# Kernel optimization log

Measured on AMD Instinct MI355X. Metric: run time of the kernel, lower is better.

The kernel has to match this reference:

```python
import jax, jax.numpy as jnp
import numpy as np

N = 100000
E = 1250000
IN_C = 64
HID = 128
OUT_C = 64
K = 10
ALPHA = 0.1


def setup_inputs() -> dict:
    key = jax.random.key(0)
    ks = jax.random.split(key, 10)
    s = 1.0 / np.sqrt(IN_C)
    sh = 1.0 / np.sqrt(HID)
    return {
        "x": jax.random.normal(ks[0], (N, IN_C), jnp.float32),
        "edge_attr": jax.random.normal(ks[1], (E, IN_C), jnp.float32),
        "W_node": jax.random.uniform(ks[2], (IN_C, HID), jnp.float32, -s, s),
        "b_node": jnp.zeros((HID,), jnp.float32),
        "W_edge": jax.random.uniform(ks[3], (IN_C, HID), jnp.float32, -s, s),
        "b_edge": jnp.zeros((HID,), jnp.float32),
        "W1": jax.random.uniform(ks[4], (HID, HID), jnp.float32, -sh, sh),
        "b1": jnp.zeros((HID,), jnp.float32),
        "W2": jax.random.uniform(ks[5], (HID, OUT_C), jnp.float32, -sh, sh),
        "b2": jnp.zeros((OUT_C,), jnp.float32),
        "edge_index": jax.random.randint(ks[6], (2, E), 0, N, jnp.int32),
    }


def _appnp(h0, edge_index):
    # PyG APPNP with gcn_norm (adds self-loops, symmetric normalization).
    src = jnp.concatenate([edge_index[0], jnp.arange(N, dtype=edge_index.dtype)])
    dst = jnp.concatenate([edge_index[1], jnp.arange(N, dtype=edge_index.dtype)])
    ew = jnp.ones(src.shape, h0.dtype)
    deg = jax.ops.segment_sum(ew, dst, num_segments=N)
    dinv = jnp.where(deg > 0, jax.lax.rsqrt(jnp.maximum(deg, 1e-12)), 0.0)
    norm = (dinv[src] * dinv[dst])[:, None]  # [(E+N),1]

    def step(h, _):
        agg = jax.ops.segment_sum(norm * h[src], dst, num_segments=N)
        return (1.0 - ALPHA) * agg + ALPHA * h0, None

    h, _ = jax.lax.scan(step, h0, None, length=K)
    return h


def reference(x, edge_attr, W_node, b_node, W_edge, b_edge, W1, b1, W2, b2, edge_index):
    x_node = x @ W_node + b_node            # [N, HID]
    e_emb = edge_attr @ W_edge + b_edge     # [E, HID]
    # add self loops with zero edge embeddings
    ar = jnp.arange(N, dtype=edge_index.dtype)
    row = jnp.concatenate([edge_index[0], ar])
    col = jnp.concatenate([edge_index[1], ar])
    e_emb_loop = jnp.concatenate([e_emb, jnp.zeros((N, HID), e_emb.dtype)], axis=0)
    msg = x_node[col] + e_emb_loop           # [(E+N), HID]
    ssum = jax.ops.segment_sum(msg, row, num_segments=N)
    cnt = jax.ops.segment_sum(jnp.ones(row.shape, x.dtype), row, num_segments=N)
    x_enh = ssum / jnp.maximum(cnt, 1.0)[:, None]  # scatter mean (cnt>=1 via loops)
    x_enh = jax.nn.relu(x_enh)               # dropout = identity in eval
    h = jax.nn.relu(x_enh @ W1 + b1)
    h0 = h @ W2 + b2                         # [N, OUT_C]
    return _appnp(h0, edge_index)
```

## Files before the change

### kernel.cpp

```cpp
#include <hip/hip_runtime.h>
#include <hip/hip_bf16.h>
#include <hip/hip_fp16.h>

#define N_NODES 100000
#define E_EDGES 1250000
#define INC 64
#define HIDC 128
#define OUTC 64
#define K_ITERS 10
#define ALPHA 0.1f

__global__ __launch_bounds__(256) void hist2(const int* __restrict__ ei,
                                             int* __restrict__ degRow,
                                             int* __restrict__ degDst) {
    int e = blockIdx.x * 256 + threadIdx.x;
    if (e >= E_EDGES) return;
    atomicAdd(&degRow[ei[e]], 1);
    atomicAdd(&degDst[ei[E_EDGES + e]], 1);
}

__global__ __launch_bounds__(256) void dinv_kernel(const int* __restrict__ degDst,
                                                   float* __restrict__ dinv) {
    int i = blockIdx.x * 256 + threadIdx.x;
    if (i >= N_NODES) return;
    dinv[i] = rsqrtf((float)(degDst[i] + 1));
}

__global__ __launch_bounds__(256) void xconvert(const float2* __restrict__ x2,
                                                __half2* __restrict__ x16) {
    int i = blockIdx.x * 256 + threadIdx.x;
    if (i >= N_NODES * 32) return;
    float2 v = x2[i];
    x16[i] = __floats2half2_rn(v.x, v.y);
}

__global__ __launch_bounds__(256) void scan_block_sums2(const int* __restrict__ degRow,
                                                        const int* __restrict__ degDst,
                                                        int* __restrict__ blockSums) {
    const int* deg = blockIdx.y ? degDst : degRow;
    __shared__ int sh[256];
    int t = threadIdx.x;
    int i = blockIdx.x * 256 + t;
    sh[t] = (i < N_NODES) ? deg[i] : 0;
    __syncthreads();
    for (int off = 128; off > 0; off >>= 1) {
        if (t < off) sh[t] += sh[t + off];
        __syncthreads();
    }
    if (t == 0) blockSums[blockIdx.y * 512 + blockIdx.x] = sh[0];
}

__global__ __launch_bounds__(512) void scan_top2(const int* __restrict__ blockSums,
                                                 int* __restrict__ blockScan, int nb) {
    const int* bs = blockSums + blockIdx.x * 512;
    int* bo = blockScan + blockIdx.x * 512;
    __shared__ int sh[512];
    int t = threadIdx.x;
    int v = (t < nb) ? bs[t] : 0;
    sh[t] = v;
    __syncthreads();
    for (int off = 1; off < 512; off <<= 1) {
        int xv = (t >= off) ? sh[t - off] : 0;
        __syncthreads();
        sh[t] += xv;
        __syncthreads();
    }
    if (t < nb) bo[t] = sh[t] - v;
}

__global__ __launch_bounds__(256) void scan_write_rp2(const int* __restrict__ degRow,
                                                      const int* __restrict__ degDst,
                                                      const int* __restrict__ blockScan,
                                                      int* __restrict__ rpRow,
                                                      int* __restrict__ rpDst) {
    const int* deg = blockIdx.y ? degDst : degRow;
    int* rp = blockIdx.y ? rpDst : rpRow;
    __shared__ int sh[256];
    int t = threadIdx.x;
    int i = blockIdx.x * 256 + t;
    int v = (i < N_NODES) ? deg[i] : 0;
    sh[t] = v;
    __syncthreads();
    for (int off = 1; off < 256; off <<= 1) {
        int xv = (t >= off) ? sh[t - off] : 0;
        __syncthreads();
        sh[t] += xv;
        __syncthreads();
    }
    if (i < N_NODES) rp[i] = blockScan[blockIdx.y * 512 + blockIdx.x] + (sh[t] - v);
    if (i == 0) rp[N_NODES] = E_EDGES;
}

__global__ __launch_bounds__(256) void scatter_both(const int* __restrict__ ei,
                                                    const float* __restrict__ dinv,
                                                    const int* __restrict__ rpRow,
                                                    const int* __restrict__ rpDst,
                                                    int* __restrict__ curRow,
                                                    int* __restrict__ curDst,
                                                    int2* __restrict__ ce,
                                                    int2* __restrict__ ew) {
    int e = blockIdx.x * 256 + threadIdx.x;
    if (e >= E_EDGES) return;
    int r0 = ei[e];
    int r1 = ei[E_EDGES + e];
    int pr = rpRow[r0] + atomicAdd(&curRow[r0], 1);
    ce[pr] = make_int2(r1, e);
    int pd = rpDst[r1] + atomicAdd(&curDst[r1], 1);
    float w = (1.0f - ALPHA) * dinv[r0] * dinv[r1];
    ew[pd] = make_int2(r0, __float_as_int(w));
}

__global__ __launch_bounds__(256) void aggregate(const float2* __restrict__ x2,
                                                 const __half2* __restrict__ x16,
                                                 const float2* __restrict__ ea2,
                                                 const int* __restrict__ rpRow,
                                                 const int2* __restrict__ ce,
                                                 float* __restrict__ S,
                                                 float* __restrict__ cntRow) {
    int wid = (blockIdx.x * 256 + threadIdx.x) >> 6;
    int lane = threadIdx.x & 63;
    if (wid >= N_NODES) return;
    int half = lane >> 5;
    int l2 = lane & 31;
    int jb = rpRow[wid], je = rpRow[wid + 1];
    float ax0 = 0.f, ay0 = 0.f, ax1 = 0.f, ay1 = 0.f;
    float ex0 = 0.f, ey0 = 0.f, ex1 = 0.f, ey1 = 0.f;
    if (!half) {
        float2 self = x2[(size_t)wid * 32 + l2];
        ax0 = self.x; ay0 = self.y;
    }
    int j = jb;
    for (; j + 3 < je; j += 4) {
        int2 c0 = ce[j + half];
        int2 c1 = ce[j + 2 + half];
        float2 xg0 = __half22float2(x16[(size_t)c0.x * 32 + l2]);
        float2 eg0 = ea2[(size_t)c0.y * 32 + l2];
        float2 xg1 = __half22float2(x16[(size_t)c1.x * 32 + l2]);
        float2 eg1 = ea2[(size_t)c1.y * 32 + l2];
        ax0 += xg0.x; ay0 += xg0.y; ex0 += eg0.x; ey0 += eg0.y;
        ax1 += xg1.x; ay1 += xg1.y; ex1 += eg1.x; ey1 += eg1.y;
    }
    for (; j < je; j += 2) {
        int ii = j + half;
        int2 c = ce[ii < je ? ii : (je - 1)];
        float m = (ii < je) ? 1.0f : 0.0f;
        float2 xg = __half22float2(x16[(size_t)c.x * 32 + l2]);
        float2 eg = ea2[(size_t)c.y * 32 + l2];
        ax0 += m * xg.x; ay0 += m * xg.y;
        ex0 += m * eg.x; ey0 += m * eg.y;
    }
    ax0 += ax1; ay0 += ay1; ex0 += ex1; ey0 += ey1;
    ax0 += __shfl_xor(ax0, 32);
    ay0 += __shfl_xor(ay0, 32);
    ex0 += __shfl_xor(ex0, 32);
    ey0 += __shfl_xor(ey0, 32);
    if (!half) {
        *reinterpret_cast<float2*>(&S[(size_t)wid * 128 + l2 * 2]) = make_float2(ax0, ay0);
        *reinterpret_cast<float2*>(&S[(size_t)wid * 128 + 64 + l2 * 2]) = make_float2(ex0, ey0);
        if (lane == 0) cntRow[wid] = (float)(je - jb + 1);
    }
}

template <int NC, int MODE>
__global__ __launch_bounds__(256) void gemm_k(const float* __restrict__ A,
                                              const float* __restrict__ Wa,
                                              const float* __restrict__ Wb,
                                              const float* __restrict__ ba,
                                              const float* __restrict__ bb,
                                              const float* __restrict__ cnt,
                                              float* __restrict__ out) {
    constexpr int CPT = NC / 16;
    __shared__ float Al[64][132];
    __shared__ float Wl[64][NC];
    const int tid = threadIdx.x;
    const int rb = blockIdx.x * 64;

    for (int idx = tid; idx < 64 * 32; idx += 256) {
        int r = idx >> 5, c4 = idx & 31;
        int gr = rb + r;
        float4 v = make_float4(0.f, 0.f, 0.f, 0.f);
        if (gr < N_NODES) v = *reinterpret_cast<const float4*>(A + (size_t)gr * 128 + c4 * 4);
        *reinterpret_cast<float4*>(&Al[r][c4 * 4]) = v;
    }

    const int trow = tid >> 4, tcol = tid & 15;
    float acc[4][CPT];
#pragma unroll
    for (int q = 0; q < 4; q++)
#pragma unroll
        for (int j = 0; j < CPT; j++) acc[q][j] = 0.f;

    for (int half = 0; half < 2; ++half) {
        __syncthreads();
        for (int idx = tid; idx < 64 * (NC / 4); idx += 256) {
            int k = idx / (NC / 4), c4 = idx % (NC / 4);
            int gk = half * 64 + k;
            const float* src;
            if constexpr (MODE == 0) {
                src = (gk < 64) ? (Wa + (size_t)gk * NC + c4 * 4)
                                : (Wb + (size_t)(gk - 64) * NC + c4 * 4);
            } else {
                src = Wa + (size_t)gk * NC + c4 * 4;
            }
            *reinterpret_cast<float4*>(&Wl[k][c4 * 4]) = *reinterpret_cast<const float4*>(src);
        }
        __syncthreads();
#pragma unroll 4
        for (int k = 0; k < 64; k++) {
            float a0 = Al[trow][half * 64 + k];
            float a1 = Al[trow + 16][half * 64 + k];
            float a2 = Al[trow + 32][half * 64 + k];
            float a3 = Al[trow + 48][half * 64 + k];
#pragma unroll
            for (int j = 0; j < CPT; j++) {
                float w = Wl[k][j * 16 + tcol];
                acc[0][j] += a0 * w;
                acc[1][j] += a1 * w;
                acc[2][j] += a2 * w;
                acc[3][j] += a3 * w;
            }
        }
    }

#pragma unroll
    for (int q = 0; q < 4; q++) {
        int gr = rb + trow + 16 * q;
        if (gr >= N_NODES) continue;
        float inv = 0.f;
        if constexpr (MODE == 0) inv = 1.0f / cnt[gr];
#pragma unroll
        for (int j = 0; j < CPT; j++) {
            int c = j * 16 + tcol;
            float v = acc[q][j];
            if constexpr (MODE == 0) {
                v = v * inv + ba[c] + (1.0f - inv) * bb[c];
                v = fmaxf(v, 0.f);
                out[(size_t)gr * NC + c] = v;
            } else if constexpr (MODE == 1) {
                v = fmaxf(v + ba[c], 0.f);
                out[(size_t)gr * NC + c] = v;
            } else {
                v = v + ba[c];
                ((__half*)out)[(size_t)gr * NC + c] = __float2half(v);
            }
        }
    }
}

template <bool LAST>
__global__ __launch_bounds__(256) void appnp_step(const __half2* __restrict__ h2,
                                                  const __half2* __restrict__ h02,
                                                  void* __restrict__ outv,
                                                  const int* __restrict__ rp,
                                                  const int2* __restrict__ ew,
                                                  const float* __restrict__ dinv) {
    int wid = (blockIdx.x * 256 + threadIdx.x) >> 6;
    int lane = threadIdx.x & 63;
    if (wid >= N_NODES) return;
    int half = lane >> 5;
    int l2 = lane & 31;
    float acc0x = 0.f, acc0y = 0.f, acc1x = 0.f, acc1y = 0.f;
    if (!half) {
        float di = dinv[wid];
        float sw = (1.0f - ALPHA) * di * di;
        float2 hv = __half22float2(h2[(size_t)wid * 32 + l2]);
        acc0x = sw * hv.x; acc0y = sw * hv.y;
    }
    int e = rp[wid], eend = rp[wid + 1];
    for (; e + 3 < eend; e += 4) {
        int2 p0 = ew[e + half];
        int2 p1 = ew[e + 2 + half];
        float w0 = __int_as_float(p0.y);
        float w1 = __int_as_float(p1.y);
        float2 g0 = __half22float2(h2[(size_t)p0.x * 32 + l2]);
        float2 g1 = __half22float2(h2[(size_t)p1.x * 32 + l2]);
        acc0x += w0 * g0.x; acc0y += w0 * g0.y;
        acc1x += w1 * g1.x; acc1y += w1 * g1.y;
    }
    for (; e < eend; e += 2) {
        int ii = e + half;
        int2 p = ew[ii < eend ? ii : (eend - 1)];
        float w0 = (ii < eend) ? __int_as_float(p.y) : 0.0f;
        float2 g = __half22float2(h2[(size_t)p.x * 32 + l2]);
        acc0x += w0 * g.x; acc0y += w0 * g.y;
    }
    acc0x += acc1x; acc0y += acc1y;
    acc0x += __shfl_xor(acc0x, 32);
    acc0y += __shfl_xor(acc0y, 32);
    if (!half) {
        float2 hz = __half22float2(h02[(size_t)wid * 32 + l2]);
        float ox = acc0x + ALPHA * hz.x;
        float oy = acc0y + ALPHA * hz.y;
        if constexpr (LAST) {
            ((float2*)outv)[(size_t)wid * 32 + l2] = make_float2(ox, oy);
        } else {
            ((__half2*)outv)[(size_t)wid * 32 + l2] = __floats2half2_rn(ox, oy);
        }
    }
}

extern "C" void kernel_launch(void* const* d_in, const int* in_sizes, int n_in,
                              void* d_out, int out_size, void* d_ws, size_t ws_size,
                              hipStream_t stream) {
    const float* x      = (const float*)d_in[0];
    const float* eattr  = (const float*)d_in[1];
    const float* W_node = (const float*)d_in[2];
    const float* b_node = (const float*)d_in[3];
    const float* W_edge = (const float*)d_in[4];
    const float* b_edge = (const float*)d_in[5];
    const float* W1     = (const float*)d_in[6];
    const float* b1     = (const float*)d_in[7];
    const float* W2     = (const float*)d_in[8];
    const float* b2     = (const float*)d_in[9];
    const int*   ei     = (const int*)d_in[10];
    float* out = (float*)d_out;

    char* ws = (char*)d_ws;
    size_t off = 0;
    auto alloc = [&](size_t bytes) -> void* {
        void* p = ws + off;
        off += (bytes + 511) & ~(size_t)511;
        return p;
    };
    float*  buf0   = (float*)alloc((size_t)N_NODES * 128 * 4);
    __half* h0_16  = (__half*)alloc((size_t)N_NODES * 64 * 2);
    __half* x16    = (__half*)alloc((size_t)N_NODES * 64 * 2);
    int2*   ew     = (int2*)alloc((size_t)E_EDGES * 8);
    float*  cntRow = (float*)alloc((size_t)N_NODES * 4);
    int*    zeros4 = (int*)alloc((size_t)4 * N_NODES * 4);
    float*  dinv   = (float*)alloc((size_t)N_NODES * 4);
    int*    rpRow  = (int*)alloc((size_t)(N_NODES + 1) * 4);
    int*    rpDst  = (int*)alloc((size_t)(N_NODES + 1) * 4);
    int*    blockSums = (int*)alloc(1024 * 4);
    int*    blockScan = (int*)alloc(1024 * 4);

    int* degRow = zeros4;
    int* degDst = zeros4 + N_NODES;
    int* curRow = zeros4 + 2 * N_NODES;
    int* curDst = zeros4 + 3 * N_NODES;

    int2* ce = (int2*)h0_16;

    constexpr int NB = (N_NODES + 255) / 256;

    hipMemsetAsync(zeros4, 0, (size_t)4 * N_NODES * 4, stream);

    hist2<<<(E_EDGES + 255) / 256, 256, 0, stream>>>(ei, degRow, degDst);
    dinv_kernel<<<(N_NODES + 255) / 256, 256, 0, stream>>>(degDst, dinv);
    xconvert<<<(N_NODES * 32 + 255) / 256, 256, 0, stream>>>((const float2*)x, (__half2*)x16);

    scan_block_sums2<<<dim3(NB, 2), 256, 0, stream>>>(degRow, degDst, blockSums);
    scan_top2<<<2, 512, 0, stream>>>(blockSums, blockScan, NB);
    scan_write_rp2<<<dim3(NB, 2), 256, 0, stream>>>(degRow, degDst, blockScan, rpRow, rpDst);

    scatter_both<<<(E_EDGES + 255) / 256, 256, 0, stream>>>(ei, dinv, rpRow, rpDst,
                                                            curRow, curDst, ce, ew);

    aggregate<<<(N_NODES + 3) / 4, 256, 0, stream>>>((const float2*)x, (const __half2*)x16,
                                                     (const float2*)eattr, rpRow, ce,
                                                     buf0, cntRow);

    gemm_k<128, 0><<<(N_NODES + 63) / 64, 256, 0, stream>>>(buf0, W_node, W_edge, b_node, b_edge, cntRow, buf0);
    gemm_k<128, 1><<<(N_NODES + 63) / 64, 256, 0, stream>>>(buf0, W1, nullptr, b1, nullptr, nullptr, buf0);
    gemm_k<64, 2><<<(N_NODES + 63) / 64, 256, 0, stream>>>(buf0, W2, nullptr, b2, nullptr, nullptr, (float*)h0_16);

    __half* hA16 = (__half*)buf0;
    __half* hB16 = (__half*)(buf0 + (size_t)N_NODES * 32);
    const __half2* hcur = (const __half2*)h0_16;
    for (int k = 0; k < K_ITERS; k++) {
        if (k == K_ITERS - 1) {
            appnp_step<true><<<(N_NODES * 64 + 255) / 256, 256, 0, stream>>>(
                hcur, (const __half2*)h0_16, (void*)out, rpDst, ew, dinv);
        } else {
            __half* dst = (k & 1) ? hB16 : hA16;
            appnp_step<false><<<(N_NODES * 64 + 255) / 256, 256, 0, stream>>>(
                hcur, (const __half2*)h0_16, (void*)dst, rpDst, ew, dinv);
            hcur = (const __half2*)dst;
        }
    }
}
```

Measured before the change: 1.097 ms.

## Replace FP32 SIMT GEMMs with FP16 MFMA kernels and half-precision intermediates

Replaces the three scalar-FMA dense layers with a matrix-core kernel built on mfma_f32_16x16x32_f16. It adds a small pre-pass that transposes and converts the weights to fp16. The aggregation output and the GEMM intermediates are now stored in half precision, which halves their memory traffic. The cost is lower precision in the MLP intermediates and three extra tiny kernel launches.

New measurement: 990.5 us (median of 2 runs). 1.11x faster.

```diff
diff --git a/kernel.cpp b/kernel.cpp
--- a/kernel.cpp
+++ b/kernel.cpp
@@ -10,6 +10,9 @@
 #define K_ITERS 10
 #define ALPHA 0.1f
 
+typedef _Float16 f16x8 __attribute__((ext_vector_type(8)));
+typedef float f32x4 __attribute__((ext_vector_type(4)));
+
 __global__ __launch_bounds__(256) void hist2(const int* __restrict__ ei,
                                              int* __restrict__ degRow,
                                              int* __restrict__ degDst) {
@@ -32,6 +35,18 @@
     if (i >= N_NODES * 32) return;
     float2 v = x2[i];
     x16[i] = __floats2half2_rn(v.x, v.y);
+}
+
+__global__ __launch_bounds__(256) void wtrans(const float* __restrict__ Wa,
+                                              const float* __restrict__ Wb,
+                                              __half* __restrict__ dst, int NC) {
+    int idx = blockIdx.x * 256 + threadIdx.x;
+    if (idx >= NC * 128) return;
+    int n = idx >> 7, k = idx & 127;
+    float v;
+    if (Wb != nullptr && k >= 64) v = Wb[(size_t)(k - 64) * NC + n];
+    else v = Wa[(size_t)k * NC + n];
+    dst[idx] = __float2half(v);
 }
 
 __global__ __launch_bounds__(256) void scan_block_sums2(const int* __restrict__ degRow,
@@ -115,7 +130,7 @@
                                                  const float2* __restrict__ ea2,
                                                  const int* __restrict__ rpRow,
                                                  const int2* __restrict__ ce,
-                                                 float* __restrict__ S,
+                                                 __half2* __restrict__ S16,
                                                  float* __restrict__ cntRow) {
     int wid = (blockIdx.x * 256 + threadIdx.x) >> 6;
     int lane = threadIdx.x & 63;
@@ -155,94 +170,82 @@
     ex0 += __shfl_xor(ex0, 32);
     ey0 += __shfl_xor(ey0, 32);
     if (!half) {
-        *reinterpret_cast<float2*>(&S[(size_t)wid * 128 + l2 * 2]) = make_float2(ax0, ay0);
-        *reinterpret_cast<float2*>(&S[(size_t)wid * 128 + 64 + l2 * 2]) = make_float2(ex0, ey0);
+        S16[(size_t)wid * 64 + l2] = __floats2half2_rn(ax0, ay0);
+        S16[(size_t)wid * 64 + 32 + l2] = __floats2half2_rn(ex0, ey0);
         if (lane == 0) cntRow[wid] = (float)(je - jb + 1);
     }
 }
 
 template <int NC, int MODE>
-__global__ __launch_bounds__(256) void gemm_k(const float* __restrict__ A,
-                                              const float* __restrict__ Wa,
-                                              const float* __restrict__ Wb,
-                                              const float* __restrict__ ba,
-                                              const float* __restrict__ bb,
-                                              const float* __restrict__ cnt,
-                                              float* __restrict__ out) {
-    constexpr int CPT = NC / 16;
-    __shared__ float Al[64][132];
-    __shared__ float Wl[64][NC];
+__global__ __launch_bounds__(256) void gemm_mfma(const __half* __restrict__ A,
+                                                 const __half* __restrict__ Wt,
+                                                 const float* __restrict__ ba,
+                                                 const float* __restrict__ bb,
+                                                 const float* __restrict__ cnt,
+                                                 __half* __restrict__ out) {
+    constexpr int NT = NC / 16;
+    __shared__ __half Ah[64][136];
+    __shared__ __half Wl[NC][136];
     const int tid = threadIdx.x;
     const int rb = blockIdx.x * 64;
-
-    for (int idx = tid; idx < 64 * 32; idx += 256) {
-        int r = idx >> 5, c4 = idx & 31;
+    const int lane = tid & 63;
+    const int wv = tid >> 6;
+    const int l15 = lane & 15;
+    const int lb = lane >> 4;
+
+    for (int idx = tid; idx < 64 * 16; idx += 256) {
+        int r = idx >> 4, c8 = idx & 15;
         int gr = rb + r;
-        float4 v = make_float4(0.f, 0.f, 0.f, 0.f);
-        if (gr < N_NODES) v = *reinterpret_cast<const float4*>(A + (size_t)gr * 128 + c4 * 4);
-        *reinterpret_cast<float4*>(&Al[r][c4 * 4]) = v;
-    }
-
-    const int trow = tid >> 4, tcol = tid & 15;
-    float acc[4][CPT];
-#pragma unroll
-    for (int q = 0; q < 4; q++)
-#pragma unroll
-        for (int j = 0; j < CPT; j++) acc[q][j] = 0.f;
-
-    for (int half = 0; half < 2; ++half) {
-        __syncthreads();
-        for (int idx = tid; idx < 64 * (NC / 4); idx += 256) {
-            int k = idx / (NC / 4), c4 = idx % (NC / 4);
-            int gk = half * 64 + k;
-            const float* src;
+        uint4 v = make_uint4(0, 0, 0, 0);
+        if (gr < N_NODES) v = *reinterpret_cast<const uint4*>(A + (size_t)gr * 128 + c8 * 8);
+        *reinterpret_cast<uint4*>(&Ah[r][c8 * 8]) = v;
+    }
+    for (int idx = tid; idx < NC * 16; idx += 256) {
+        int n = idx >> 4, c8 = idx & 15;
+        uint4 v = *reinterpret_cast<const uint4*>(Wt + (size_t)n * 128 + c8 * 8);
+        *reinterpret_cast<uint4*>(&Wl[n][c8 * 8]) = v;
+    }
+    __syncthreads();
+
+    f16x8 af[4];
+#pragma unroll
+    for (int kc = 0; kc < 4; kc++)
+        af[kc] = *reinterpret_cast<const f16x8*>(&Ah[wv * 16 + l15][kc * 32 + lb * 8]);
+
+    f32x4 acc[NT];
+#pragma unroll
+    for (int nt = 0; nt < NT; nt++) acc[nt] = (f32x4){0.f, 0.f, 0.f, 0.f};
+
+#pragma unroll
+    for (int nt = 0; nt < NT; nt++) {
+#pragma unroll
+        for (int kc = 0; kc < 4; kc++) {
+            f16x8 bf = *reinterpret_cast<const f16x8*>(&Wl[nt * 16 + l15][kc * 32 + lb * 8]);
+            acc[nt] = __builtin_amdgcn_mfma_f32_16x16x32_f16(af[kc], bf, acc[nt], 0, 0, 0);
+        }
+    }
+
+#pragma unroll
+    for (int nt = 0; nt < NT; nt++) {
+        int c = nt * 16 + l15;
+        float bav = ba[c];
+        float bbv = 0.f;
+        if constexpr (MODE == 0) bbv = bb[c];
+#pragma unroll
+        for (int reg = 0; reg < 4; reg++) {
+            int gr = rb + wv * 16 + lb * 4 + reg;
+            if (gr >= N_NODES) continue;
+            float v = acc[nt][reg];
             if constexpr (MODE == 0) {
-                src = (gk < 64) ? (Wa + (size_t)gk * NC + c4 * 4)
-                                : (Wb + (size_t)(gk - 64) * NC + c4 * 4);
+                float inv = 1.0f / cnt[gr];
+                v = v * inv + bav + (1.0f - inv) * bbv;
+                v = fmaxf(v, 0.f);
+            } else if constexpr (MODE == 1) {
+                v = fmaxf(v + bav, 0.f);
             } else {
-                src = Wa + (size_t)gk * NC + c4 * 4;
+                v = v + bav;
             }
-            *reinterpret_cast<float4*>(&Wl[k][c4 * 4]) = *reinterpret_cast<const float4*>(src);
-        }
-        __syncthreads();
-#pragma unroll 4
-        for (int k = 0; k < 64; k++) {
-            float a0 = Al[trow][half * 64 + k];
-            float a1 = Al[trow + 16][half * 64 + k];
-            float a2 = Al[trow + 32][half * 64 + k];
-            float a3 = Al[trow + 48][half * 64 + k];
-#pragma unroll
-            for (int j = 0; j < CPT; j++) {
-                float w = Wl[k][j * 16 + tcol];
-                acc[0][j] += a0 * w;
-                acc[1][j] += a1 * w;
-                acc[2][j] += a2 * w;
-                acc[3][j] += a3 * w;
-            }
-        }
-    }
-
-#pragma unroll
-    for (int q = 0; q < 4; q++) {
-        int gr = rb + trow + 16 * q;
-        if (gr >= N_NODES) continue;
-        float inv = 0.f;
-        if constexpr (MODE == 0) inv = 1.0f / cnt[gr];
-#pragma unroll
-        for (int j = 0; j < CPT; j++) {
-            int c = j * 16 + tcol;
-            float v = acc[q][j];
-            if constexpr (MODE == 0) {
-                v = v * inv + ba[c] + (1.0f - inv) * bb[c];
-                v = fmaxf(v, 0.f);
-                out[(size_t)gr * NC + c] = v;
-            } else if constexpr (MODE == 1) {
-                v = fmaxf(v + ba[c], 0.f);
-                out[(size_t)gr * NC + c] = v;
-            } else {
-                v = v + ba[c];
-                ((__half*)out)[(size_t)gr * NC + c] = __float2half(v);
-            }
+            out[(size_t)gr * NC + c] = __float2half(v);
         }
     }
 }
@@ -333,6 +336,9 @@
     int*    rpDst  = (int*)alloc((size_t)(N_NODES + 1) * 4);
     int*    blockSums = (int*)alloc(1024 * 4);
     int*    blockScan = (int*)alloc(1024 * 4);
+    __half* wt0    = (__half*)alloc((size_t)128 * 128 * 2);
+    __half* wt1    = (__half*)alloc((size_t)128 * 128 * 2);
+    __half* wt2    = (__half*)alloc((size_t)64 * 128 * 2);
 
     int* degRow = zeros4;
     int* degDst = zeros4 + N_NODES;
@@ -340,6 +346,7 @@
     int* curDst = zeros4 + 3 * N_NODES;
 
     int2* ce = (int2*)h0_16;
+    __half* S16 = (__half*)buf0;
 
     constexpr int NB = (N_NODES + 255) / 256;
 
@@ -348,6 +355,9 @@
     hist2<<<(E_EDGES + 255) / 256, 256, 0, stream>>>(ei, degRow, degDst);
     dinv_kernel<<<(N_NODES + 255) / 256, 256, 0, stream>>>(degDst, dinv);
     xconvert<<<(N_NODES * 32 + 255) / 256, 256, 0, stream>>>((const float2*)x, (__half2*)x16);
+    wtrans<<<64, 256, 0, stream>>>(W_node, W_edge, wt0, 128);
+    wtrans<<<64, 256, 0, stream>>>(W1, nullptr, wt1, 128);
+    wtrans<<<32, 256, 0, stream>>>(W2, nullptr, wt2, 64);
 
     scan_block_sums2<<<dim3(NB, 2), 256, 0, stream>>>(degRow, degDst, blockSums);
     scan_top2<<<2, 512, 0, stream>>>(blockSums, blockScan, NB);
@@ -358,21 +368,22 @@
 
     aggregate<<<(N_NODES + 3) / 4, 256, 0, stream>>>((const float2*)x, (const __half2*)x16,
                                                      (const float2*)eattr, rpRow, ce,
-                                                     buf0, cntRow);
-
-    gemm_k<128, 0><<<(N_NODES + 63) / 64, 256, 0, stream>>>(buf0, W_node, W_edge, b_node, b_edge, cntRow, buf0);
-    gemm_k<128, 1><<<(N_NODES + 63) / 64, 256, 0, stream>>>(buf0, W1, nullptr, b1, nullptr, nullptr, buf0);
-    gemm_k<64, 2><<<(N_NODES + 63) / 64, 256, 0, stream>>>(buf0, W2, nullptr, b2, nullptr, nullptr, (float*)h0_16);
-
-    __half* hA16 = (__half*)buf0;
-    __half* hB16 = (__half*)(buf0 + (size_t)N_NODES * 32);
+                                                     (__half2*)S16, cntRow);
+
+    constexpr int GB = (N_NODES + 63) / 64;
+    gemm_mfma<128, 0><<<GB, 256, 0, stream>>>(S16, wt0, b_node, b_edge, cntRow, S16);
+    gemm_mfma<128, 1><<<GB, 256, 0, stream>>>(S16, wt1, b1, nullptr, nullptr, S16);
+    gemm_mfma<64, 2><<<GB, 256, 0, stream>>>(S16, wt2, b2, nullptr, nullptr, h0_16);
+
+    __half2* hA16 = (__half2*)buf0;
+    __half2* hB16 = (__half2*)(buf0 + (size_t)N_NODES * 32);
     const __half2* hcur = (const __half2*)h0_16;
     for (int k = 0; k < K_ITERS; k++) {
         if (k == K_ITERS - 1) {
             appnp_step<true><<<(N_NODES * 64 + 255) / 256, 256, 0, stream>>>(
                 hcur, (const __half2*)h0_16, (void*)out, rpDst, ew, dinv);
         } else {
-            __half* dst = (k & 1) ? hB16 : hA16;
+            __half2* dst = (k & 1) ? hB16 : hA16;
             appnp_step<false><<<(N_NODES * 64 + 255) / 256, 256, 0, stream>>>(
                 hcur, (const __half2*)h0_16, (void*)dst, rpDst, ew, dinv);
             hcur = (const __half2*)dst;
```
